# Optimization experiments

Measured on AMD Instinct MI355X. Metric: run time of the kernel, lower is better.

Reference implementation:

```python
import jax, jax.numpy as jnp
import numpy as np

B, N, D = 2, 2048, 1024          # batch, query tokens, model dim
NC, DC = 77, 768                 # context tokens, context dim (CLIP)
H, DH = 16, 64                   # heads, head dim (H*DH == D)
FF = 4 * D                       # GEGLU inner dim
SCALE = DH ** -0.5
EPS = 1e-5


def setup_inputs() -> dict:
    key = jax.random.key(0)
    ks = iter(jax.random.split(key, 32))
    rn = lambda *s: jax.random.normal(next(ks), s, dtype=jnp.float32) * 0.02
    inp = {
        'x': jax.random.normal(next(ks), (B, N, D), dtype=jnp.float32),
        'context': jax.random.normal(next(ks), (B, NC, DC), dtype=jnp.float32),
        # attn1 (self-attention): all projections from dim D
        'w1_q': rn(D, D), 'w1_k': rn(D, D), 'w1_v': rn(D, D),
        'w1_o': rn(D, D), 'b1_o': jnp.zeros((D,), jnp.float32),
        # attn2 (cross-attention): k/v from context dim DC
        'w2_q': rn(D, D), 'w2_k': rn(DC, D), 'w2_v': rn(DC, D),
        'w2_o': rn(D, D), 'b2_o': jnp.zeros((D,), jnp.float32),
        # layernorms
        'ln1_g': jnp.ones((D,), jnp.float32), 'ln1_b': jnp.zeros((D,), jnp.float32),
        'ln2_g': jnp.ones((D,), jnp.float32), 'ln2_b': jnp.zeros((D,), jnp.float32),
        'ln3_g': jnp.ones((D,), jnp.float32), 'ln3_b': jnp.zeros((D,), jnp.float32),
        # GEGLU feed-forward: proj -> 2*FF (value, gate), then FF -> D
        'ff_w1': rn(D, 2 * FF), 'ff_b1': jnp.zeros((2 * FF,), jnp.float32),
        'ff_w2': rn(FF, D), 'ff_b2': jnp.zeros((D,), jnp.float32),
    }
    return inp


def _layer_norm(x, g, b):
    mu = jnp.mean(x, axis=-1, keepdims=True)
    var = jnp.mean(jnp.square(x - mu), axis=-1, keepdims=True)
    return (x - mu) * jax.lax.rsqrt(var + EPS) * g + b


def _attention(xq, ctx, wq, wk, wv, wo, bo):
    b, n, _ = xq.shape
    m = ctx.shape[1]
    q = (xq @ wq).reshape(b, n, H, DH)
    k = (ctx @ wk).reshape(b, m, H, DH)
    v = (ctx @ wv).reshape(b, m, H, DH)
    sim = jnp.einsum('bihd,bjhd->bhij', q, k) * SCALE
    attn = jax.nn.softmax(sim, axis=-1)
    out = jnp.einsum('bhij,bjhd->bihd', attn, v).reshape(b, n, H * DH)
    return out @ wo + bo


def reference(x, context,
              w1_q, w1_k, w1_v, w1_o, b1_o,
              w2_q, w2_k, w2_v, w2_o, b2_o,
              ln1_g, ln1_b, ln2_g, ln2_b, ln3_g, ln3_b,
              ff_w1, ff_b1, ff_w2, ff_b2):
    # self-attention + residual
    h = _layer_norm(x, ln1_g, ln1_b)
    x = _attention(h, h, w1_q, w1_k, w1_v, w1_o, b1_o) + x
    # cross-attention + residual
    h = _layer_norm(x, ln2_g, ln2_b)
    x = _attention(h, context, w2_q, w2_k, w2_v, w2_o, b2_o) + x
    # GEGLU feed-forward + residual (torch F.gelu is exact erf)
    h = _layer_norm(x, ln3_g, ln3_b)
    p = h @ ff_w1 + ff_b1
    val, gate = p[..., :FF], p[..., FF:]
    x = (val * jax.nn.gelu(gate, approximate=False)) @ ff_w2 + ff_b2 + x
    return x
```

## Files before the change

kernel.cpp:

```cpp
#include <hip/hip_runtime.h>
#include <hip/hip_bf16.h>
#include <math.h>

#define B_    2
#define N_    2048
#define D_    1024
#define NC_   77
#define DC_   768
#define H_    16
#define DH_   64
#define FF_   4096
#define EPS_  1e-5f
#define SCALE_ 0.125f
#define NEG_BIG -1e30f

typedef __attribute__((ext_vector_type(8))) short short8;
typedef __attribute__((ext_vector_type(4))) float f32x4;
#define MFMA16(a, b, c) __builtin_amdgcn_mfma_f32_16x16x32_bf16(a, b, c, 0, 0, 0)

static __device__ __forceinline__ unsigned short f2bf_raw(float f) {
    union { float f; unsigned int i; } x; x.f = f;
    unsigned int r = x.i + 0x7fffu + ((x.i >> 16) & 1u);
    return (unsigned short)(r >> 16);
}

static __device__ __forceinline__ void gload16(const void* g, void* l) {
    __builtin_amdgcn_global_load_lds(
        (const __attribute__((address_space(1))) void*)g,
        (__attribute__((address_space(3))) void*)l, 16, 0, 0);
}

__global__ __launch_bounds__(256) void wtrans_k(const float* __restrict__ src,
                                                unsigned short* __restrict__ dst,
                                                int K, int N) {
    __shared__ unsigned short t[64][68];
    const int k0 = blockIdx.y * 64, n0 = blockIdx.x * 64;
    const int rr = threadIdx.x >> 4;
    const int cc = (threadIdx.x & 15) * 4;
#pragma unroll
    for (int p = 0; p < 4; p++) {
        int k = rr + p * 16;
        float4 vd = *(const float4*)&src[(size_t)(k0 + k) * N + n0 + cc];
        t[k][cc + 0] = f2bf_raw(vd.x); t[k][cc + 1] = f2bf_raw(vd.y);
        t[k][cc + 2] = f2bf_raw(vd.z); t[k][cc + 3] = f2bf_raw(vd.w);
    }
    __syncthreads();
#pragma unroll
    for (int p = 0; p < 4; p++) {
        int n = rr + p * 16;
        ushort4 o;
        o.x = t[cc + 0][n]; o.y = t[cc + 1][n];
        o.z = t[cc + 2][n]; o.w = t[cc + 3][n];
        *(ushort4*)&dst[(size_t)(n0 + n) * K + k0 + cc] = o;
    }
}

__global__ __launch_bounds__(256) void ln_k(const float* __restrict__ x,
                                            const float* __restrict__ g,
                                            const float* __restrict__ b,
                                            unsigned short* __restrict__ out) {
    int row = blockIdx.x;
    const float* xr = x + (size_t)row * D_;
    float v0[4]; float s = 0.f, sq = 0.f;
#pragma unroll
    for (int i = 0; i < 4; i++) {
        float t = xr[threadIdx.x + 256 * i];
        v0[i] = t; s += t; sq += t * t;
    }
#pragma unroll
    for (int off = 32; off; off >>= 1) {
        s  += __shfl_xor(s,  off);
        sq += __shfl_xor(sq, off);
    }
    __shared__ float rs[4], rq[4];
    int wave = threadIdx.x >> 6, lane = threadIdx.x & 63;
    if (lane == 0) { rs[wave] = s; rq[wave] = sq; }
    __syncthreads();
    s  = rs[0] + rs[1] + rs[2] + rs[3];
    sq = rq[0] + rq[1] + rq[2] + rq[3];
    float mu  = s * (1.f / D_);
    float var = sq * (1.f / D_) - mu * mu;
    float inv = rsqrtf(var + EPS_);
#pragma unroll
    for (int i = 0; i < 4; i++) {
        int c = threadIdx.x + 256 * i;
        out[(size_t)row * D_ + c] = f2bf_raw((v0[i] - mu) * inv * g[c] + b[c]);
    }
}

__global__ __launch_bounds__(256) void gemm_mfma_k(
        const unsigned short* __restrict__ A,
        const unsigned short* __restrict__ BT,
        const float* __restrict__ bias,
        const float* __restrict__ res,
        float* __restrict__ outf,
        unsigned short* __restrict__ oq,
        unsigned short* __restrict__ ok,
        unsigned short* __restrict__ ov,
        int M, int N, int K, int mode) {
    __shared__ unsigned short As[128 * 32];
    __shared__ unsigned short Bs[128 * 32];
    const int tid = threadIdx.x;
    const int w = tid >> 6, lane = tid & 63, quad = lane >> 4, l15 = lane & 15;
    const int wm = w >> 1, wn = w & 1;
    const int m0 = blockIdx.y * 128, n0 = blockIdx.x * 128;
    const int srow = lane >> 2;
    const int schunk = lane & 3;
    const int kswz = (schunk ^ (srow & 3)) * 8;
    const int rdsw = (quad ^ (l15 & 3)) * 8;

    f32x4 acc[4][4] = {};
    for (int k0 = 0; k0 < K; k0 += 32) {
#pragma unroll
        for (int i = 0; i < 2; i++) {
            int r = (w * 2 + i) * 16;
            gload16(&A[(size_t)(m0 + r + srow) * K + k0 + kswz], &As[r * 32]);
            gload16(&BT[(size_t)(n0 + r + srow) * K + k0 + kswz], &Bs[r * 32]);
        }
        __syncthreads();
        short8 af[4], bf[4];
#pragma unroll
        for (int i = 0; i < 4; i++) {
            af[i] = *(const short8*)&As[(wm * 64 + i * 16 + l15) * 32 + rdsw];
            bf[i] = *(const short8*)&Bs[(wn * 64 + i * 16 + l15) * 32 + rdsw];
        }
#pragma unroll
        for (int i = 0; i < 4; i++)
#pragma unroll
            for (int j = 0; j < 4; j++)
                acc[i][j] = MFMA16(af[i], bf[j], acc[i][j]);
        __syncthreads();
    }
#pragma unroll
    for (int i = 0; i < 4; i++) {
#pragma unroll
        for (int r = 0; r < 4; r++) {
            const int row = m0 + wm * 64 + i * 16 + quad * 4 + r;
#pragma unroll
            for (int j = 0; j < 4; j++) {
                const int col = n0 + wn * 64 + j * 16 + l15;
                float c = acc[i][j][r];
                if (mode == 0) {
                    int which = col >> 10, cc = col & 1023;
                    unsigned short* dst = which == 0 ? oq : (which == 1 ? ok : ov);
                    dst[(size_t)row * 1024 + cc] = f2bf_raw(which == 0 ? c * SCALE_ : c);
                } else {
                    outf[(size_t)row * N + col] =
                        c + bias[col] + res[(size_t)row * N + col];
                }
            }
        }
    }
}

__global__ __launch_bounds__(256) void gemm64_k(
        const unsigned short* __restrict__ A,
        const unsigned short* __restrict__ BT,
        const float* __restrict__ bias,
        const float* __restrict__ res,
        float* __restrict__ outf,
        unsigned short* __restrict__ outb,
        float scale,
        int M, int N, int K, int mode) {
    __shared__ unsigned short As[64 * 64];
    __shared__ unsigned short Bs[64 * 64];
    const int tid = threadIdx.x;
    const int w = tid >> 6, lane = tid & 63, quad = lane >> 4, l15 = lane & 15;
    const int wm = w >> 1, wn = w & 1;
    const int m0 = blockIdx.y * 64, n0 = blockIdx.x * 64;
    const int sr8 = lane >> 3;
    const int sc8 = lane & 7;

    f32x4 acc[2][2] = {};
    for (int k0 = 0; k0 < K; k0 += 64) {
#pragma unroll
        for (int i = 0; i < 2; i++) {
            int row = w * 16 + i * 8 + sr8;
            int gch = sc8 ^ (row & 7);
            gload16(&A[(size_t)(m0 + row) * K + k0 + gch * 8], &As[(w * 16 + i * 8) * 64]);
            gload16(&BT[(size_t)(n0 + row) * K + k0 + gch * 8], &Bs[(w * 16 + i * 8) * 64]);
        }
        __syncthreads();
        short8 af[2][2], bf[2][2];
#pragma unroll
        for (int ii = 0; ii < 2; ii++) {
            int ra = wm * 32 + ii * 16 + l15;
            int rb = wn * 32 + ii * 16 + l15;
#pragma unroll
            for (int kh = 0; kh < 2; kh++) {
                int ca = (kh * 4 + quad) ^ (ra & 7);
                int cb = (kh * 4 + quad) ^ (rb & 7);
                af[ii][kh] = *(const short8*)&As[ra * 64 + ca * 8];
                bf[ii][kh] = *(const short8*)&Bs[rb * 64 + cb * 8];
            }
        }
#pragma unroll
        for (int ii = 0; ii < 2; ii++)
#pragma unroll
            for (int jj = 0; jj < 2; jj++) {
                acc[ii][jj] = MFMA16(af[ii][0], bf[jj][0], acc[ii][jj]);
                acc[ii][jj] = MFMA16(af[ii][1], bf[jj][1], acc[ii][jj]);
            }
        __syncthreads();
    }
#pragma unroll
    for (int ii = 0; ii < 2; ii++) {
#pragma unroll
        for (int r = 0; r < 4; r++) {
            const int row = m0 + wm * 32 + ii * 16 + quad * 4 + r;
#pragma unroll
            for (int jj = 0; jj < 2; jj++) {
                const int col = n0 + wn * 32 + jj * 16 + l15;
                float c = acc[ii][jj][r];
                if (mode == 0) {
                    outb[(size_t)row * N + col] = f2bf_raw(c * scale);
                } else {
                    outf[(size_t)row * N + col] =
                        c + bias[col] + res[(size_t)row * N + col];
                }
            }
        }
    }
}

__global__ __launch_bounds__(256, 4) void geglu_mfma_k(
        const unsigned short* __restrict__ A,
        const unsigned short* __restrict__ BT,
        const float* __restrict__ bias,
        unsigned short* __restrict__ outg,
        int M, int K) {
    __shared__ unsigned short As[64 * 64];
    __shared__ unsigned short Bv[128 * 64];
    __shared__ unsigned short Bg[128 * 64];
    const int tid = threadIdx.x;
    const int w = tid >> 6, lane = tid & 63, quad = lane >> 4, l15 = lane & 15;
    const int m0 = blockIdx.y * 64, n0 = blockIdx.x * 128;
    const int sr8 = lane >> 3, sc8 = lane & 7;

    f32x4 accv[4][2] = {}, accg[4][2] = {};
    for (int k0 = 0; k0 < K; k0 += 64) {
#pragma unroll
        for (int i = 0; i < 2; i++) {
            int row = w * 16 + i * 8 + sr8;
            int gch = sc8 ^ (row & 7);
            gload16(&A[(size_t)(m0 + row) * K + k0 + gch * 8], &As[(w * 16 + i * 8) * 64]);
        }
#pragma unroll
        for (int i = 0; i < 4; i++) {
            int row = w * 32 + i * 8 + sr8;
            int gch = sc8 ^ (row & 7);
            gload16(&BT[(size_t)(n0 + row) * K + k0 + gch * 8], &Bv[(w * 32 + i * 8) * 64]);
            gload16(&BT[(size_t)(FF_ + n0 + row) * K + k0 + gch * 8], &Bg[(w * 32 + i * 8) * 64]);
        }
        __syncthreads();
        short8 af[4][2];
#pragma unroll
        for (int ii = 0; ii < 4; ii++) {
            int ra = ii * 16 + l15;
#pragma unroll
            for (int kh = 0; kh < 2; kh++) {
                int ca = (kh * 4 + quad) ^ (ra & 7);
                af[ii][kh] = *(const short8*)&As[ra * 64 + ca * 8];
            }
        }
#pragma unroll
        for (int jj = 0; jj < 2; jj++) {
            const int rb = w * 32 + jj * 16 + l15;
            const int c0 = (0 * 4 + quad) ^ (rb & 7);
            const int c1 = (1 * 4 + quad) ^ (rb & 7);
            const short8 bv0 = *(const short8*)&Bv[rb * 64 + c0 * 8];
            const short8 bv1 = *(const short8*)&Bv[rb * 64 + c1 * 8];
            const short8 bg0 = *(const short8*)&Bg[rb * 64 + c0 * 8];
            const short8 bg1 = *(const short8*)&Bg[rb * 64 + c1 * 8];
#pragma unroll
            for (int ii = 0; ii < 4; ii++) {
                accv[ii][jj] = MFMA16(af[ii][0], bv0, accv[ii][jj]);
                accv[ii][jj] = MFMA16(af[ii][1], bv1, accv[ii][jj]);
                accg[ii][jj] = MFMA16(af[ii][0], bg0, accg[ii][jj]);
                accg[ii][jj] = MFMA16(af[ii][1], bg1, accg[ii][jj]);
            }
        }
        __syncthreads();
    }
#pragma unroll
    for (int ii = 0; ii < 4; ii++) {
#pragma unroll
        for (int r = 0; r < 4; r++) {
            const int row = m0 + ii * 16 + quad * 4 + r;
#pragma unroll
            for (int jj = 0; jj < 2; jj++) {
                const int col = n0 + w * 32 + jj * 16 + l15;
                float vv = accv[ii][jj][r] + bias[col];
                float gg = accg[ii][jj][r] + bias[col + FF_];
                float ge = 0.5f * gg * (1.f + erff(gg * 0.70710678118654752f));
                outg[(size_t)row * FF_ + col] = f2bf_raw(vv * ge);
            }
        }
    }
}

__global__ __launch_bounds__(256) void gemm_k(const float* __restrict__ A,
                                              const float* __restrict__ W,
                                              unsigned short* __restrict__ outb,
                                              int M, int N, int K) {
    __shared__ float As[16][64];
    __shared__ float Ws[16][64];
    const int tx = threadIdx.x & 15;
    const int ty = threadIdx.x >> 4;
    const int m0 = blockIdx.y * 64, n0 = blockIdx.x * 64;
    const int lm = threadIdx.x >> 2;
    const int lk = (threadIdx.x & 3) * 4;
    const int wr = threadIdx.x >> 4;
    const int wc = (threadIdx.x & 15) * 4;
    float acc[4][4] = {};
    for (int k0 = 0; k0 < K; k0 += 16) {
        float4 av = make_float4(0.f, 0.f, 0.f, 0.f);
        if (m0 + lm < M) av = *(const float4*)&A[(size_t)(m0 + lm) * K + k0 + lk];
        float4 wv = *(const float4*)&W[(size_t)(k0 + wr) * N + n0 + wc];
        As[lk + 0][lm] = av.x; As[lk + 1][lm] = av.y;
        As[lk + 2][lm] = av.z; As[lk + 3][lm] = av.w;
        *(float4*)&Ws[wr][wc] = wv;
        __syncthreads();
#pragma unroll
        for (int kk = 0; kk < 16; kk++) {
            float4 a = *(const float4*)&As[kk][ty * 4];
            float4 b = *(const float4*)&Ws[kk][tx * 4];
            float ar[4] = { a.x, a.y, a.z, a.w };
            float br[4] = { b.x, b.y, b.z, b.w };
#pragma unroll
            for (int i = 0; i < 4; i++)
#pragma unroll
                for (int j = 0; j < 4; j++)
                    acc[i][j] = fmaf(ar[i], br[j], acc[i][j]);
        }
        __syncthreads();
    }
#pragma unroll
    for (int i = 0; i < 4; i++) {
        int row = m0 + ty * 4 + i;
        if (row >= M) continue;
        ushort4 u;
        u.x = f2bf_raw(acc[i][0]); u.y = f2bf_raw(acc[i][1]);
        u.z = f2bf_raw(acc[i][2]); u.w = f2bf_raw(acc[i][3]);
        *(ushort4*)&outb[(size_t)row * N + n0 + tx * 4] = u;
    }
}

__global__ __launch_bounds__(256) void vtrans_k(const unsigned short* __restrict__ v,
                                                unsigned short* __restrict__ vT,
                                                int ntok, int tokrows, int npad) {
    __shared__ unsigned short tile[64][68];
    const int bh = blockIdx.x, b = bh >> 4, h = bh & 15;
    const int t0 = blockIdx.y * 64;
    const int tt = threadIdx.x >> 4;
    const int dg = (threadIdx.x & 15) * 4;
#pragma unroll
    for (int p = 0; p < 4; p++) {
        int tok = t0 + tt + 16 * p;
        ushort4 val = make_ushort4(0, 0, 0, 0);
        if (tok < ntok)
            val = *(const ushort4*)&v[((size_t)(b * tokrows + tok)) * D_ + h * DH_ + dg];
        *(ushort4*)&tile[tt + 16 * p][dg] = val;
    }
    __syncthreads();
#pragma unroll
    for (int p = 0; p < 4; p++) {
        int d = tt + 16 * p;
        ushort4 w;
        w.x = tile[dg + 0][d]; w.y = tile[dg + 1][d];
        w.z = tile[dg + 2][d]; w.w = tile[dg + 3][d];
        *(ushort4*)&vT[((size_t)(bh * 64 + d)) * npad + t0 + dg] = w;
    }
}

__global__ __launch_bounds__(256, 4) void flash2_k(
        const unsigned short* __restrict__ qb,
        const unsigned short* __restrict__ kb,
        const unsigned short* __restrict__ vT,
        unsigned short* __restrict__ o,
        int n_kv, int kv_rows, int npadv, int ntiles) {
    __shared__ unsigned short Ks[2][64 * 64];
    __shared__ unsigned short Vs[2][64 * 64];
    __shared__ unsigned short Pls[4][16 * 64];
    const int bh = blockIdx.x, b = bh >> 4, h = bh & 15;
    const int w = threadIdx.x >> 6;
    const int lane = threadIdx.x & 63, quad = lane >> 4, l15 = lane & 15;
    const int q0 = blockIdx.y * 64 + w * 16;

    const size_t qoff = ((size_t)(b * N_ + q0 + l15)) * D_ + h * DH_ + quad * 8;
    const short8 qf0 = *(const short8*)&qb[qoff];
    const short8 qf1 = *(const short8*)&qb[qoff + 32];

    short8 onesf;
#pragma unroll
    for (int i = 0; i < 8; i++) onesf[i] = (short)0x3F80;

    const int sr = lane >> 3;
    const int sc = lane & 7;
    const unsigned short* vbase = vT + (size_t)(bh * 64) * npadv;

    auto stage = [&](int buf, int t) {
        const int j0 = t * 64;
#pragma unroll
        for (int i = 0; i < 2; i++) {
            const int row = w * 16 + i * 8 + sr;
            const int gch = (sc ^ (row & 7)) * 8;
            gload16(&kb[(size_t)(b * kv_rows + j0 + row) * D_ + h * DH_ + gch],
                    &Ks[buf][(w * 16 + i * 8) * 64]);
            gload16(&vbase[(size_t)row * npadv + j0 + gch],
                    &Vs[buf][(w * 16 + i * 8) * 64]);
        }
    };

    f32x4 O0 = {0.f, 0.f, 0.f, 0.f}, O1 = O0, O2 = O0, O3 = O0, L4 = O0;

    stage(0, 0);
    __syncthreads();

    for (int t = 0; t < ntiles; t++) {
        const int cur = t & 1;
        if (t + 1 < ntiles) stage(cur ^ 1, t + 1);
        const int j0 = t * 64;

        f32x4 s[4];
        __builtin_amdgcn_s_setprio(1);
#pragma unroll
        for (int cb = 0; cb < 4; cb++) {
            const int ra = 16 * cb + l15;
            const int sw = ra & 7;
            const short8 k0 = *(const short8*)&Ks[cur][ra * 64 + ((quad ^ sw) * 8)];
            const short8 k1 = *(const short8*)&Ks[cur][ra * 64 + (((quad + 4) ^ sw) * 8)];
            f32x4 z = {0.f, 0.f, 0.f, 0.f};
            z = MFMA16(qf0, k0, z);
            z = MFMA16(qf1, k1, z);
            s[cb] = z;
        }
        __builtin_amdgcn_s_setprio(0);
        if (j0 + 64 > n_kv) {
#pragma unroll
            for (int cb = 0; cb < 4; cb++)
                if (j0 + 16 * cb + l15 >= n_kv) {
                    s[cb][0] = NEG_BIG; s[cb][1] = NEG_BIG;
                    s[cb][2] = NEG_BIG; s[cb][3] = NEG_BIG;
                }
        }

#pragma unroll
        for (int cb = 0; cb < 4; cb++) {
            const int lc = (l15 >> 3) + 2 * cb;
            const int e = l15 & 7;
#pragma unroll
            for (int r = 0; r < 4; r++) {
                const int pr = quad * 4 + r;
                Pls[w][pr * 64 + ((lc ^ (pr & 7)) * 8 + e)] =
                    f2bf_raw(__expf(s[cb][r]));
            }
        }
        const int psw = l15 & 7;
        const short8 pf0 = *(const short8*)&Pls[w][l15 * 64 + ((quad ^ psw) * 8)];
        const short8 pf1 = *(const short8*)&Pls[w][l15 * 64 + (((quad + 4) ^ psw) * 8)];

        short8 vf[4][2];
#pragma unroll
        for (int n = 0; n < 4; n++) {
            const int rv = 16 * n + l15;
            const int vw = rv & 7;
            vf[n][0] = *(const short8*)&Vs[cur][rv * 64 + ((quad ^ vw) * 8)];
            vf[n][1] = *(const short8*)&Vs[cur][rv * 64 + (((quad + 4) ^ vw) * 8)];
        }
        __builtin_amdgcn_s_setprio(1);
        O0 = MFMA16(pf0, vf[0][0], O0); O0 = MFMA16(pf1, vf[0][1], O0);
        O1 = MFMA16(pf0, vf[1][0], O1); O1 = MFMA16(pf1, vf[1][1], O1);
        O2 = MFMA16(pf0, vf[2][0], O2); O2 = MFMA16(pf1, vf[2][1], O2);
        O3 = MFMA16(pf0, vf[3][0], O3); O3 = MFMA16(pf1, vf[3][1], O3);
        L4 = MFMA16(pf0, onesf, L4);    L4 = MFMA16(pf1, onesf, L4);
        __builtin_amdgcn_s_setprio(0);

        __syncthreads();
    }

    const size_t obase = ((size_t)(b * N_ + q0 + quad * 4)) * D_ + h * DH_ + l15;
#pragma unroll
    for (int r = 0; r < 4; r++) {
        const float inv = 1.0f / L4[r];
        unsigned short* orow = &o[obase + (size_t)r * D_];
        orow[0]  = f2bf_raw(O0[r] * inv);
        orow[16] = f2bf_raw(O1[r] * inv);
        orow[32] = f2bf_raw(O2[r] * inv);
        orow[48] = f2bf_raw(O3[r] * inv);
    }
}

extern "C" void kernel_launch(void* const* d_in, const int* in_sizes, int n_in,
                              void* d_out, int out_size, void* d_ws, size_t ws_size,
                              hipStream_t stream) {
    const float* x_in  = (const float*)d_in[0];
    const float* ctx_in= (const float*)d_in[1];
    const float* w1q = (const float*)d_in[2];
    const float* w1k = (const float*)d_in[3];
    const float* w1v = (const float*)d_in[4];
    const float* w1o = (const float*)d_in[5];
    const float* b1o = (const float*)d_in[6];
    const float* w2q = (const float*)d_in[7];
    const float* w2k = (const float*)d_in[8];
    const float* w2v = (const float*)d_in[9];
    const float* w2o = (const float*)d_in[10];
    const float* b2o = (const float*)d_in[11];
    const float* ln1g= (const float*)d_in[12];
    const float* ln1b= (const float*)d_in[13];
    const float* ln2g= (const float*)d_in[14];
    const float* ln2b= (const float*)d_in[15];
    const float* ln3g= (const float*)d_in[16];
    const float* ln3b= (const float*)d_in[17];
    const float* ffw1= (const float*)d_in[18];
    const float* ffb1= (const float*)d_in[19];
    const float* ffw2= (const float*)d_in[20];
    const float* ffb2= (const float*)d_in[21];
    float* out_f = (float*)d_out;

    char* ws = (char*)d_ws;
    unsigned short* wqkvT = (unsigned short*)(ws);
    unsigned short* w1oT  = (unsigned short*)(ws + (size_t)( 6 << 20));
    unsigned short* w2qT  = (unsigned short*)(ws + (size_t)( 8 << 20));
    unsigned short* w2oT  = (unsigned short*)(ws + (size_t)(10 << 20));
    unsigned short* ffw1T = (unsigned short*)(ws + (size_t)(12 << 20));
    unsigned short* ffw2T = (unsigned short*)(ws + (size_t)(28 << 20));
    float*          xbuf  = (float*)         (ws + (size_t)(36 << 20));
    unsigned short* h     = (unsigned short*)(ws + (size_t)(52 << 20));
    unsigned short* qb    = (unsigned short*)(ws + (size_t)(60 << 20));
    unsigned short* kb    = (unsigned short*)(ws + (size_t)(68 << 20));
    unsigned short* vTb   = (unsigned short*)(ws + (size_t)(76 << 20));
    unsigned short* vb    = (unsigned short*)(ws + (size_t)(84 << 20));
    unsigned short* g     = (unsigned short*)(ws + (size_t)(60 << 20));

    const int MT = B_ * N_;

    auto wt = [&](const float* src, unsigned short* dst, int K, int N) {
        hipLaunchKernelGGL(wtrans_k, dim3(N / 64, K / 64), dim3(256), 0, stream, src, dst, K, N);
    };
    auto gmm = [&](const unsigned short* A, const unsigned short* BT,
                   const float* bias, const float* res, float* outf,
                   unsigned short* oq, unsigned short* ok, unsigned short* ov,
                   int M, int N, int K, int mode) {
        hipLaunchKernelGGL(gemm_mfma_k, dim3(N / 128, M / 128), dim3(256), 0, stream,
                           A, BT, bias, res, outf, oq, ok, ov, M, N, K, mode);
    };
    auto g64 = [&](const unsigned short* A, const unsigned short* BT,
                   const float* bias, const float* res, float* outf,
                   unsigned short* outb, float scale, int M, int N, int K, int mode) {
        hipLaunchKernelGGL(gemm64_k, dim3(N / 64, M / 64), dim3(256), 0, stream,
                           A, BT, bias, res, outf, outb, scale, M, N, K, mode);
    };

    wt(w1q, wqkvT,                 D_, D_);
    wt(w1k, wqkvT + (1024 * 1024), D_, D_);
    wt(w1v, wqkvT + (2048 * 1024), D_, D_);
    wt(w1o, w1oT, D_, D_);
    wt(w2q, w2qT, D_, D_);
    wt(w2o, w2oT, D_, D_);
    wt(ffw1, ffw1T, D_, 2 * FF_);
    wt(ffw2, ffw2T, FF_, D_);

    hipLaunchKernelGGL(ln_k, dim3(MT), dim3(256), 0, stream, x_in, ln1g, ln1b, h);
    gmm(h, wqkvT, nullptr, nullptr, nullptr, qb, kb, vb, MT, 3072, D_, 0);
    hipLaunchKernelGGL(vtrans_k, dim3(B_ * H_, N_ / 64), dim3(256), 0, stream,
                       vb, vTb, N_, N_, N_);
    hipLaunchKernelGGL(flash2_k, dim3(B_ * H_, N_ / 64), dim3(256), 0, stream,
                       qb, kb, vTb, vb , N_, N_, N_, N_ / 64);
    g64(vb , w1oT, b1o, x_in, xbuf, nullptr, 1.0f, MT, D_, D_, 1);

    hipLaunchKernelGGL(ln_k, dim3(MT), dim3(256), 0, stream, xbuf, ln2g, ln2b, h);
    g64(h, w2qT, nullptr, nullptr, nullptr, qb, SCALE_, MT, D_, D_, 0);
    hipLaunchKernelGGL(gemm_k, dim3(D_ / 64, 3), dim3(256), 0, stream,
                       ctx_in, w2k, kb, B_ * NC_, D_, DC_);
    hipLaunchKernelGGL(gemm_k, dim3(D_ / 64, 3), dim3(256), 0, stream,
                       ctx_in, w2v, vb, B_ * NC_, D_, DC_);
    hipLaunchKernelGGL(vtrans_k, dim3(B_ * H_, 2), dim3(256), 0, stream,
                       vb, vTb, NC_, NC_, 128);
    hipLaunchKernelGGL(flash2_k, dim3(B_ * H_, N_ / 64), dim3(256), 0, stream,
                       qb, kb, vTb, vb , NC_, NC_, 128, 2);
    g64(vb , w2oT, b2o, xbuf, xbuf, nullptr, 1.0f, MT, D_, D_, 1);

    hipLaunchKernelGGL(ln_k, dim3(MT), dim3(256), 0, stream, xbuf, ln3g, ln3b, h);
    hipLaunchKernelGGL(geglu_mfma_k, dim3(FF_ / 128, MT / 64), dim3(256), 0, stream,
                       h, ffw1T, ffb1, g, MT, D_);
    g64(g, ffw2T, ffb2, xbuf, out_f, nullptr, 1.0f, MT, D_, FF_, 1);
}
```

Baseline: 619.9 us.

## Batch six weight transposes into one launch, use fast erf, precompute GEMM load pointers

```diff
diff --git a/kernel.cpp b/kernel.cpp
--- a/kernel.cpp
+++ b/kernel.cpp
@@ -24,6 +24,19 @@
     return (unsigned short)(r >> 16);
 }
 
+static __device__ __forceinline__ float erf_fast(float x) {
+    const float ax = fabsf(x);
+    const float t = __frcp_rn(fmaf(0.3275911f, ax, 1.0f));
+    float p = fmaf(1.061405429f, t, -1.453152027f);
+    p = fmaf(p, t, 1.421413741f);
+    p = fmaf(p, t, -0.284496736f);
+    p = fmaf(p, t, 0.254829592f);
+    p = p * t;
+    const float e = __expf(-ax * ax);
+    float r = fmaf(-p, e, 1.0f);
+    return copysignf(r, x);
+}
+
 static __device__ __forceinline__ void gload16(const void* g, void* l) {
     __builtin_amdgcn_global_load_lds(
         (const __attribute__((address_space(1))) void*)g,
@@ -48,6 +61,33 @@
 #pragma unroll
     for (int p = 0; p < 4; p++) {
         int n = rr + p * 16;
+        ushort4 o;
+        o.x = t[cc + 0][n]; o.y = t[cc + 1][n];
+        o.z = t[cc + 2][n]; o.w = t[cc + 3][n];
+        *(ushort4*)&dst[(size_t)(n0 + n) * K + k0 + cc] = o;
+    }
+}
+
+struct WT6 { const float* s[6]; unsigned short* d[6]; };
+__global__ __launch_bounds__(256) void wtrans6_k(WT6 p) {
+    __shared__ unsigned short t[64][68];
+    const float* __restrict__ src = p.s[blockIdx.z];
+    unsigned short* __restrict__ dst = p.d[blockIdx.z];
+    const int K = 1024, N = 1024;
+    const int k0 = blockIdx.y * 64, n0 = blockIdx.x * 64;
+    const int rr = threadIdx.x >> 4;
+    const int cc = (threadIdx.x & 15) * 4;
+#pragma unroll
+    for (int pq = 0; pq < 4; pq++) {
+        int k = rr + pq * 16;
+        float4 vd = *(const float4*)&src[(size_t)(k0 + k) * N + n0 + cc];
+        t[k][cc + 0] = f2bf_raw(vd.x); t[k][cc + 1] = f2bf_raw(vd.y);
+        t[k][cc + 2] = f2bf_raw(vd.z); t[k][cc + 3] = f2bf_raw(vd.w);
+    }
+    __syncthreads();
+#pragma unroll
+    for (int pq = 0; pq < 4; pq++) {
+        int n = rr + pq * 16;
         ushort4 o;
         o.x = t[cc + 0][n]; o.y = t[cc + 1][n];
         o.z = t[cc + 2][n]; o.w = t[cc + 3][n];
@@ -109,13 +149,23 @@
     const int kswz = (schunk ^ (srow & 3)) * 8;
     const int rdsw = (quad ^ (l15 & 3)) * 8;
 
+    const unsigned short* pA[2];
+    const unsigned short* pB[2];
+#pragma unroll
+    for (int i = 0; i < 2; i++) {
+        int r = (w * 2 + i) * 16;
+        pA[i] = &A[(size_t)(m0 + r + srow) * K + kswz];
+        pB[i] = &BT[(size_t)(n0 + r + srow) * K + kswz];
+    }
+
     f32x4 acc[4][4] = {};
     for (int k0 = 0; k0 < K; k0 += 32) {
 #pragma unroll
         for (int i = 0; i < 2; i++) {
             int r = (w * 2 + i) * 16;
-            gload16(&A[(size_t)(m0 + r + srow) * K + k0 + kswz], &As[r * 32]);
-            gload16(&BT[(size_t)(n0 + r + srow) * K + k0 + kswz], &Bs[r * 32]);
+            gload16(pA[i], &As[r * 32]);
+            gload16(pB[i], &Bs[r * 32]);
+            pA[i] += 32; pB[i] += 32;
         }
         __syncthreads();
         short8 af[4], bf[4];
@@ -171,14 +221,23 @@
     const int sr8 = lane >> 3;
     const int sc8 = lane & 7;
 
+    const unsigned short* pA[2];
+    const unsigned short* pB[2];
+#pragma unroll
+    for (int i = 0; i < 2; i++) {
+        int row = w * 16 + i * 8 + sr8;
+        int gch = sc8 ^ (row & 7);
+        pA[i] = &A[(size_t)(m0 + row) * K + gch * 8];
+        pB[i] = &BT[(size_t)(n0 + row) * K + gch * 8];
+    }
+
     f32x4 acc[2][2] = {};
     for (int k0 = 0; k0 < K; k0 += 64) {
 #pragma unroll
         for (int i = 0; i < 2; i++) {
-            int row = w * 16 + i * 8 + sr8;
-            int gch = sc8 ^ (row & 7);
-            gload16(&A[(size_t)(m0 + row) * K + k0 + gch * 8], &As[(w * 16 + i * 8) * 64]);
-            gload16(&BT[(size_t)(n0 + row) * K + k0 + gch * 8], &Bs[(w * 16 + i * 8) * 64]);
+            gload16(pA[i], &As[(w * 16 + i * 8) * 64]);
+            gload16(pB[i], &Bs[(w * 16 + i * 8) * 64]);
+            pA[i] += 64; pB[i] += 64;
         }
         __syncthreads();
         short8 af[2][2], bf[2][2];
@@ -292,7 +351,7 @@
                 const int col = n0 + w * 32 + jj * 16 + l15;
                 float vv = accv[ii][jj][r] + bias[col];
                 float gg = accg[ii][jj][r] + bias[col + FF_];
-                float ge = 0.5f * gg * (1.f + erff(gg * 0.70710678118654752f));
+                float ge = 0.5f * gg * (1.f + erf_fast(gg * 0.70710678118654752f));
                 outg[(size_t)row * FF_ + col] = f2bf_raw(vv * ge);
             }
         }
@@ -552,12 +611,14 @@
                            A, BT, bias, res, outf, outb, scale, M, N, K, mode);
     };
 
-    wt(w1q, wqkvT,                 D_, D_);
-    wt(w1k, wqkvT + (1024 * 1024), D_, D_);
-    wt(w1v, wqkvT + (2048 * 1024), D_, D_);
-    wt(w1o, w1oT, D_, D_);
-    wt(w2q, w2qT, D_, D_);
-    wt(w2o, w2oT, D_, D_);
+    WT6 wt6;
+    wt6.s[0] = w1q; wt6.d[0] = wqkvT;
+    wt6.s[1] = w1k; wt6.d[1] = wqkvT + (1024 * 1024);
+    wt6.s[2] = w1v; wt6.d[2] = wqkvT + (2048 * 1024);
+    wt6.s[3] = w1o; wt6.d[3] = w1oT;
+    wt6.s[4] = w2q; wt6.d[4] = w2qT;
+    wt6.s[5] = w2o; wt6.d[5] = w2oT;
+    hipLaunchKernelGGL(wtrans6_k, dim3(16, 16, 6), dim3(256), 0, stream, wt6);
     wt(ffw1, ffw1T, D_, 2 * FF_);
     wt(ffw2, ffw2T, FF_, D_);
 
```

New measurement: 611.2 us. About the same (-1.4%).
